# Performance work log

Hardware: AMD Instinct MI355X
Metric: run time of the kernel (lower is better)

## Reference

```python
import jax, jax.numpy as jnp
import numpy as np

B, T, A = 64, 100, 8732          # batch, padded GT boxes per image, SSD300 anchors
NUM_CLASSES = 21                 # VOC
THR = 0.5                        # overlap_threshold
VAR0, VAR1 = 0.1, 0.2            # loc_variance


def setup_inputs() -> dict:
    key = jax.random.key(0)
    k1, k2, k3, k4, k5 = jax.random.split(key, 5)
    # GT boxes: valid point-coord boxes in [0,1] with positive area, plus float label col
    xy1 = jax.random.uniform(k1, (B, T, 2)) * 0.7
    wh = jax.random.uniform(k2, (B, T, 2)) * 0.28 + 0.02
    labels = jax.random.randint(k3, (B, T), 0, NUM_CLASSES - 1).astype(jnp.float32)
    targets = jnp.concatenate([xy1, xy1 + wh, labels[..., None]], axis=-1)  # [B,T,5]
    # anchors in center coords (cx, cy, w, h), positive w/h
    cxy = jax.random.uniform(k4, (A, 2))
    awh = jax.random.uniform(k5, (A, 2)) * 0.48 + 0.02
    anchors = jnp.concatenate([cxy, awh], axis=-1)  # [A,4]
    return {"targets": targets, "anchors": anchors}


def _iou(boxes, anchors_pt):
    # boxes [T,4] point coords, anchors_pt [A,4] point coords -> [T,A]
    tl = jnp.maximum(boxes[:, None, :2], anchors_pt[None, :, :2])
    br = jnp.minimum(boxes[:, None, 2:], anchors_pt[None, :, 2:])
    inter = jnp.prod(jnp.clip(br - tl, 0.0), axis=-1)
    area_b = jnp.prod(boxes[:, 2:] - boxes[:, :2], axis=-1)
    area_a = jnp.prod(anchors_pt[:, 2:] - anchors_pt[:, :2], axis=-1)
    return inter / (area_b[:, None] + area_a[None, :] - inter)


def reference(targets, anchors):
    # centerCoordsToPointCoords(anchors)
    anchors_pt = jnp.concatenate(
        [anchors[:, :2] - anchors[:, 2:] * 0.5, anchors[:, :2] + anchors[:, 2:] * 0.5],
        axis=-1,
    )

    def match(tgt):  # tgt: [T,5]
        boxes = tgt[:, :4]
        labels = tgt[:, 4]
        iou = _iou(boxes, anchors_pt)                    # [T,A]
        anchor_index = jnp.argmax(iou, axis=1)           # best anchor per GT [T]
        gt_overlap = jnp.max(iou, axis=0)                # best GT overlap per anchor [A]
        gt_index = jnp.argmax(iou, axis=0)               # best GT per anchor [A]
        # index_fill_: guarantee each GT's best anchor counts as matched
        gt_overlap = gt_overlap.at[anchor_index].set(1.0)
        gt_index = gt_index.at[anchor_index].set(jnp.arange(boxes.shape[0]))
        matched = boxes[gt_index]                        # [A,4] point coords
        # pointCoordsToCenterCoords + encodeCenterCoords
        cxy = (matched[:, :2] + matched[:, 2:]) * 0.5
        wh = matched[:, 2:] - matched[:, :2]
        loc = jnp.concatenate(
            [(cxy - anchors[:, :2]) / (VAR0 * anchors[:, 2:]),
             jnp.log(wh / anchors[:, 2:]) / VAR1],
            axis=-1,
        )                                                # [A,4]
        conf = (labels[gt_index] + 1.0).astype(jnp.int32)
        conf = jnp.where(gt_overlap < THR, 0, conf)      # background below threshold
        return loc, conf

    return jax.vmap(match)(targets)  # loc_t [B,A,4], conf_t [B,A]
```

## Files before the change

### kernel.cpp

```cpp
#include <hip/hip_runtime.h>

#define BB 64
#define TT 100
#define TSPLIT 52
#define AA 8732
#define CHUNK 512
#define NCHUNK ((AA + CHUNK - 1) / CHUNK)

typedef unsigned long long u64;
typedef unsigned int u32;
typedef unsigned short u16;

__device__ __forceinline__ float fdiv_faithful(float i, float u) {
    float r = __builtin_amdgcn_rcpf(u);
    r = __builtin_fmaf(__builtin_fmaf(-u, r, 1.0f), r, r);
    float q = __fmul_rn(i, r);
    float rem = __builtin_fmaf(-u, q, i);
    return __builtin_fmaf(rem, r, q);
}

__device__ __forceinline__ float iou_f(float bx1, float by1, float bx2, float by2, float areab,
                                       float ax1, float ay1, float ax2, float ay2, float areaa) {
    float dx = fmaxf(__fsub_rn(fminf(bx2, ax2), fmaxf(bx1, ax1)), 0.0f);
    float dy = fmaxf(__fsub_rn(fminf(by2, ay2), fmaxf(by1, ay1)), 0.0f);
    float inter = __fmul_rn(dx, dy);
    float uni = __fsub_rn(__fadd_rn(areab, areaa), inter);
    return fdiv_faithful(inter, uni);
}

__device__ __forceinline__ void wave_max63_x4(float& x0, float& x1, float& x2, float& x3) {
#define DPP4(ctrl)                                                                              \
    {                                                                                           \
        int t0 = __builtin_amdgcn_update_dpp(__float_as_int(x0), __float_as_int(x0), (ctrl), 0xf, 0xf, false); \
        int t1 = __builtin_amdgcn_update_dpp(__float_as_int(x1), __float_as_int(x1), (ctrl), 0xf, 0xf, false); \
        int t2 = __builtin_amdgcn_update_dpp(__float_as_int(x2), __float_as_int(x2), (ctrl), 0xf, 0xf, false); \
        int t3 = __builtin_amdgcn_update_dpp(__float_as_int(x3), __float_as_int(x3), (ctrl), 0xf, 0xf, false); \
        x0 = fmaxf(x0, __int_as_float(t0));                                                     \
        x1 = fmaxf(x1, __int_as_float(t1));                                                     \
        x2 = fmaxf(x2, __int_as_float(t2));                                                     \
        x3 = fmaxf(x3, __int_as_float(t3));                                                     \
    }
    DPP4(0x111)
    DPP4(0x112)
    DPP4(0x114)
    DPP4(0x118)
    DPP4(0x142)
    DPP4(0x143)
#undef DPP4
}

__global__ __launch_bounds__(256) void k_init(u64* __restrict__ keys) {
    int i = blockIdx.x * 256 + threadIdx.x;
    if (i < BB * TT) keys[i] = 0ULL;
}

__global__ __launch_bounds__(512) void k_phaseA(const float* __restrict__ targets,
                                                const float* __restrict__ anchors,
                                                u64* __restrict__ keys,
                                                u16* __restrict__ pa) {
    const int b = blockIdx.y;
    const int tid = threadIdx.x;
    const int half = tid >> 8;
    const int u = tid & 255;
    const int a0 = blockIdx.x * CHUNK + u * 2;
    const bool valid = a0 < AA;
    const int lane = tid & 63, wv = tid >> 6;

    __shared__ float4 sh_box[TT];
    __shared__ __align__(16) float sh_area[TT];
    __shared__ u64 sh_red[4][TT];
    __shared__ u64 sh_pa[CHUNK];

    if (tid < TT) {
        const float* tg = targets + ((size_t)b * TT + tid) * 5;
        float x1 = tg[0], y1 = tg[1], x2 = tg[2], y2 = tg[3];
        sh_box[tid] = make_float4(x1, y1, x2, y2);
        sh_area[tid] = __fmul_rn(__fsub_rn(x2, x1), __fsub_rn(y2, y1));
    }
    __syncthreads();

    float ax10 = 0.f, ay10 = 0.f, ax20 = 0.f, ay20 = 0.f, aa0 = 1.f;
    float ax11 = 0.f, ay11 = 0.f, ax21 = 0.f, ay21 = 0.f, aa1 = 1.f;
    if (valid) {
        const float4* anc = (const float4*)(anchors + (size_t)a0 * 4);
        float4 c0 = anc[0], c1 = anc[1];
        float hx0 = __fmul_rn(c0.z, 0.5f), hy0 = __fmul_rn(c0.w, 0.5f);
        ax10 = __fsub_rn(c0.x, hx0); ay10 = __fsub_rn(c0.y, hy0);
        ax20 = __fadd_rn(c0.x, hx0); ay20 = __fadd_rn(c0.y, hy0);
        aa0 = __fmul_rn(__fsub_rn(ax20, ax10), __fsub_rn(ay20, ay10));
        float hx1 = __fmul_rn(c1.z, 0.5f), hy1 = __fmul_rn(c1.w, 0.5f);
        ax11 = __fsub_rn(c1.x, hx1); ay11 = __fsub_rn(c1.y, hy1);
        ax21 = __fadd_rn(c1.x, hx1); ay21 = __fadd_rn(c1.y, hy1);
        aa1 = __fmul_rn(__fsub_rn(ax21, ax11), __fsub_rn(ay21, ay11));
    }

    float best0 = -1.f, best1 = -1.f;
    int gi0 = 0, gi1 = 0;
    const u32 wave_base = (u32)blockIdx.x * CHUNK + (u32)(wv & 3) * 128u;

    const int tbeg = half ? TSPLIT : 0;
    const int tend = half ? TT : TSPLIT;
    for (int t = tbeg; t < tend; t += 4) {
        float4 B0 = sh_box[t + 0], B1 = sh_box[t + 1];
        float4 B2 = sh_box[t + 2], B3 = sh_box[t + 3];
        const float4 arv = *(const float4*)&sh_area[t];
        float ar0 = arv.x, ar1 = arv.y, ar2 = arv.z, ar3 = arv.w;

        float v00 = iou_f(B0.x, B0.y, B0.z, B0.w, ar0, ax10, ay10, ax20, ay20, aa0);
        float v01 = iou_f(B0.x, B0.y, B0.z, B0.w, ar0, ax11, ay11, ax21, ay21, aa1);
        float v10 = iou_f(B1.x, B1.y, B1.z, B1.w, ar1, ax10, ay10, ax20, ay20, aa0);
        float v11 = iou_f(B1.x, B1.y, B1.z, B1.w, ar1, ax11, ay11, ax21, ay21, aa1);
        float v20 = iou_f(B2.x, B2.y, B2.z, B2.w, ar2, ax10, ay10, ax20, ay20, aa0);
        float v21 = iou_f(B2.x, B2.y, B2.z, B2.w, ar2, ax11, ay11, ax21, ay21, aa1);
        float v30 = iou_f(B3.x, B3.y, B3.z, B3.w, ar3, ax10, ay10, ax20, ay20, aa0);
        float v31 = iou_f(B3.x, B3.y, B3.z, B3.w, ar3, ax11, ay11, ax21, ay21, aa1);

        if (v00 > best0) { best0 = v00; gi0 = t; }
        if (v10 > best0) { best0 = v10; gi0 = t + 1; }
        if (v20 > best0) { best0 = v20; gi0 = t + 2; }
        if (v30 > best0) { best0 = v30; gi0 = t + 3; }
        if (v01 > best1) { best1 = v01; gi1 = t; }
        if (v11 > best1) { best1 = v11; gi1 = t + 1; }
        if (v21 > best1) { best1 = v21; gi1 = t + 2; }
        if (v31 > best1) { best1 = v31; gi1 = t + 3; }

        float vm0 = fmaxf(v00, v01), vm1 = fmaxf(v10, v11);
        float vm2 = fmaxf(v20, v21), vm3 = fmaxf(v30, v31);
        float w0 = vm0, w1 = vm1, w2 = vm2, w3 = vm3;
        wave_max63_x4(w0, w1, w2, w3);
        u32 wm0 = (u32)__builtin_amdgcn_readlane(__float_as_int(w0), 63);
        u32 wm1 = (u32)__builtin_amdgcn_readlane(__float_as_int(w1), 63);
        u32 wm2 = (u32)__builtin_amdgcn_readlane(__float_as_int(w2), 63);
        u32 wm3 = (u32)__builtin_amdgcn_readlane(__float_as_int(w3), 63);
        u64 me0 = __ballot(vm0 == __uint_as_float(wm0));
        u64 mp0 = __ballot(v01 > v00);
        u64 me1 = __ballot(vm1 == __uint_as_float(wm1));
        u64 mp1 = __ballot(v11 > v10);
        u64 me2 = __ballot(vm2 == __uint_as_float(wm2));
        u64 mp2 = __ballot(v21 > v20);
        u64 me3 = __ballot(vm3 == __uint_as_float(wm3));
        u64 mp3 = __ballot(v31 > v30);
        u32 wl0 = (u32)(__ffsll((long long)me0) - 1);
        u32 wl1 = (u32)(__ffsll((long long)me1) - 1);
        u32 wl2 = (u32)(__ffsll((long long)me2) - 1);
        u32 wl3 = (u32)(__ffsll((long long)me3) - 1);
        u32 g0 = wave_base + wl0 * 2u + (u32)((mp0 >> wl0) & 1ULL);
        u32 g1 = wave_base + wl1 * 2u + (u32)((mp1 >> wl1) & 1ULL);
        u32 g2 = wave_base + wl2 * 2u + (u32)((mp2 >> wl2) & 1ULL);
        u32 g3 = wave_base + wl3 * 2u + (u32)((mp3 >> wl3) & 1ULL);
        if (lane == 0) {
            u64* r = &sh_red[wv & 3][t];
            r[0] = (((u64)wm0) << 32) | (u32)~g0;
            r[1] = (((u64)wm1) << 32) | (u32)~g1;
            r[2] = (((u64)wm2) << 32) | (u32)~g2;
            r[3] = (((u64)wm3) << 32) | (u32)~g3;
        }
    }
    __syncthreads();

    if (tid < TT) {
        u64 m0 = sh_red[0][tid], m1 = sh_red[1][tid];
        u64 m2 = sh_red[2][tid], m3 = sh_red[3][tid];
        u64 m = m0 > m1 ? m0 : m1;
        if (m2 > m) m = m2;
        if (m3 > m) m = m3;
        atomicMax(&keys[b * TT + tid], m);
    }

    if (half == 0) {
        sh_pa[u * 2 + 0] = (((u64)__float_as_uint(best0)) << 32) | (u32)(~(u32)gi0);
        sh_pa[u * 2 + 1] = (((u64)__float_as_uint(best1)) << 32) | (u32)(~(u32)gi1);
    }
    __syncthreads();
    if (half == 1 && valid) {
        u64 k0 = (((u64)__float_as_uint(best0)) << 32) | (u32)(~(u32)gi0);
        u64 k1 = (((u64)__float_as_uint(best1)) << 32) | (u32)(~(u32)gi1);
        u64 m0 = sh_pa[u * 2 + 0]; if (k0 > m0) m0 = k0;
        u64 m1 = sh_pa[u * 2 + 1]; if (k1 > m1) m1 = k1;
        u32 gA0 = (~(u32)m0) & 0x7Fu;
        u32 gA1 = (~(u32)m1) & 0x7Fu;
        float bv0 = __uint_as_float((u32)(m0 >> 32));
        float bv1 = __uint_as_float((u32)(m1 >> 32));
        u32 f0 = gA0 | (bv0 >= 0.5f ? 0x80u : 0u);
        u32 f1 = gA1 | (bv1 >= 0.5f ? 0x80u : 0u);
        *(u32*)(pa + (size_t)b * AA + a0) = f0 | (f1 << 16);
    }
}

__global__ __launch_bounds__(256) void k_encode(const float* __restrict__ targets,
                                                const float* __restrict__ anchors,
                                                const u64* __restrict__ keys,
                                                const u16* __restrict__ pa,
                                                float* __restrict__ out) {
    const int b = blockIdx.y;
    const int a = blockIdx.x * 256 + threadIdx.x;

    __shared__ float sh_t[TT][6];
    __shared__ u32 sh_ov[256];

    sh_ov[threadIdx.x] = 0;
    __syncthreads();
    for (int t = threadIdx.x; t < TT; t += 256) {
        const float* tg = targets + ((size_t)b * TT + t) * 5;
        sh_t[t][0] = tg[0]; sh_t[t][1] = tg[1];
        sh_t[t][2] = tg[2]; sh_t[t][3] = tg[3];
        sh_t[t][4] = tg[4];
        u32 at = ~(u32)(keys[b * TT + t] & 0xFFFFFFFFu);
        if ((at >> 8) == (u32)blockIdx.x)
            atomicMax(&sh_ov[at & 255], 0x100u | (u32)t);
    }
    __syncthreads();
    if (a >= AA) return;

    u32 ov = sh_ov[threadIdx.x];
    u32 v = pa[(size_t)b * AA + a];
    int gi; bool pos;
    if (ov) { gi = (int)(ov & 0x7F); pos = true; }
    else     { gi = (int)(v & 0x7F); pos = (v & 0x80) != 0; }

    const float4 anc = *(const float4*)(anchors + (size_t)a * 4);
    const float mx1 = sh_t[gi][0], my1 = sh_t[gi][1], mx2 = sh_t[gi][2], my2 = sh_t[gi][3];
    const float cx = (mx1 + mx2) * 0.5f, cy = (my1 + my2) * 0.5f;
    const float w = mx2 - mx1, h = my2 - my1;
    const float l0 = (cx - anc.x) / (0.1f * anc.z);
    const float l1 = (cy - anc.y) / (0.1f * anc.w);
    const float l2 = logf(w / anc.z) / 0.2f;
    const float l3 = logf(h / anc.w) / 0.2f;

    const size_t base = ((size_t)b * AA + a) * 4;
    *(float4*)(out + base) = make_float4(l0, l1, l2, l3);
    float conf = pos ? (float)(int)(sh_t[gi][4] + 1.0f) : 0.0f;
    out[(size_t)BB * AA * 4 + (size_t)b * AA + a] = conf;
}

extern "C" void kernel_launch(void* const* d_in, const int* in_sizes, int n_in,
                              void* d_out, int out_size, void* d_ws, size_t ws_size,
                              hipStream_t stream) {
    const float* targets = (const float*)d_in[0];
    const float* anchors = (const float*)d_in[1];
    float* out = (float*)d_out;
    u64* keys = (u64*)d_ws;
    u16* pa = (u16*)((char*)d_ws + (size_t)BB * TT * 8);

    k_init<<<(BB * TT + 255) / 256, 256, 0, stream>>>(keys);
    dim3 gA(NCHUNK, BB);
    k_phaseA<<<gA, 512, 0, stream>>>(targets, anchors, keys, pa);
    dim3 gE((AA + 255) / 256, BB);
    k_encode<<<gE, 256, 0, stream>>>(targets, anchors, keys, pa, out);
}
```

Before: 122.5 us.

## Split GT-box range across a second grid dimension and merge partial argmax in encode

```diff
diff --git a/kernel.cpp b/kernel.cpp
--- a/kernel.cpp
+++ b/kernel.cpp
@@ -2,7 +2,6 @@
 
 #define BB 64
 #define TT 100
-#define TSPLIT 52
 #define AA 8732
 #define CHUNK 512
 #define NCHUNK ((AA + CHUNK - 1) / CHUNK)
@@ -10,6 +9,8 @@
 typedef unsigned long long u64;
 typedef unsigned int u32;
 typedef unsigned short u16;
+
+__constant__ int c_tbl[5] = {0, 28, 52, 76, 100};
 
 __device__ __forceinline__ float fdiv_faithful(float i, float u) {
     float r = __builtin_amdgcn_rcpf(u);
@@ -57,8 +58,9 @@
 __global__ __launch_bounds__(512) void k_phaseA(const float* __restrict__ targets,
                                                 const float* __restrict__ anchors,
                                                 u64* __restrict__ keys,
-                                                u16* __restrict__ pa) {
+                                                u64* __restrict__ pa2) {
     const int b = blockIdx.y;
+    const int z = blockIdx.z;
     const int tid = threadIdx.x;
     const int half = tid >> 8;
     const int u = tid & 255;
@@ -98,8 +100,8 @@
     int gi0 = 0, gi1 = 0;
     const u32 wave_base = (u32)blockIdx.x * CHUNK + (u32)(wv & 3) * 128u;
 
-    const int tbeg = half ? TSPLIT : 0;
-    const int tend = half ? TT : TSPLIT;
+    const int tbeg = c_tbl[z * 2 + half];
+    const int tend = c_tbl[z * 2 + half + 1];
     for (int t = tbeg; t < tend; t += 4) {
         float4 B0 = sh_box[t + 0], B1 = sh_box[t + 1];
         float4 B2 = sh_box[t + 2], B3 = sh_box[t + 3];
@@ -158,7 +160,7 @@
     }
     __syncthreads();
 
-    if (tid < TT) {
+    if (tid >= c_tbl[z * 2] && tid < c_tbl[z * 2 + 2]) {
         u64 m0 = sh_red[0][tid], m1 = sh_red[1][tid];
         u64 m2 = sh_red[2][tid], m3 = sh_red[3][tid];
         u64 m = m0 > m1 ? m0 : m1;
@@ -177,21 +179,16 @@
         u64 k1 = (((u64)__float_as_uint(best1)) << 32) | (u32)(~(u32)gi1);
         u64 m0 = sh_pa[u * 2 + 0]; if (k0 > m0) m0 = k0;
         u64 m1 = sh_pa[u * 2 + 1]; if (k1 > m1) m1 = k1;
-        u32 gA0 = (~(u32)m0) & 0x7Fu;
-        u32 gA1 = (~(u32)m1) & 0x7Fu;
-        float bv0 = __uint_as_float((u32)(m0 >> 32));
-        float bv1 = __uint_as_float((u32)(m1 >> 32));
-        u32 f0 = gA0 | (bv0 >= 0.5f ? 0x80u : 0u);
-        u32 f1 = gA1 | (bv1 >= 0.5f ? 0x80u : 0u);
-        *(u32*)(pa + (size_t)b * AA + a0) = f0 | (f1 << 16);
+        pa2[((size_t)b * AA + a0) * 2 + z] = m0;
+        pa2[((size_t)b * AA + a0 + 1) * 2 + z] = m1;
     }
 }
 
 __global__ __launch_bounds__(256) void k_encode(const float* __restrict__ targets,
                                                 const float* __restrict__ anchors,
                                                 const u64* __restrict__ keys,
-                                                const u16* __restrict__ pa,
-                                                float* __restrict__ out) {
+                                                const u64* pa2,
+                                                float* out) {
     const int b = blockIdx.y;
     const int a = blockIdx.x * 256 + threadIdx.x;
 
@@ -212,11 +209,17 @@
     __syncthreads();
     if (a >= AA) return;
 
+    const u64* pc = pa2 + ((size_t)b * AA + a) * 2;
+    u64 kz0 = pc[0], kz1 = pc[1];
+    u64 m = kz0 > kz1 ? kz0 : kz1;
+
     u32 ov = sh_ov[threadIdx.x];
-    u32 v = pa[(size_t)b * AA + a];
     int gi; bool pos;
     if (ov) { gi = (int)(ov & 0x7F); pos = true; }
-    else     { gi = (int)(v & 0x7F); pos = (v & 0x80) != 0; }
+    else {
+        gi = (int)((~(u32)m) & 0x7F);
+        pos = __uint_as_float((u32)(m >> 32)) >= 0.5f;
+    }
 
     const float4 anc = *(const float4*)(anchors + (size_t)a * 4);
     const float mx1 = sh_t[gi][0], my1 = sh_t[gi][1], mx2 = sh_t[gi][2], my2 = sh_t[gi][3];
@@ -240,11 +243,11 @@
     const float* anchors = (const float*)d_in[1];
     float* out = (float*)d_out;
     u64* keys = (u64*)d_ws;
-    u16* pa = (u16*)((char*)d_ws + (size_t)BB * TT * 8);
+    u64* pa2 = (u64*)d_out;
 
     k_init<<<(BB * TT + 255) / 256, 256, 0, stream>>>(keys);
-    dim3 gA(NCHUNK, BB);
-    k_phaseA<<<gA, 512, 0, stream>>>(targets, anchors, keys, pa);
+    dim3 gA(NCHUNK, BB, 2);
+    k_phaseA<<<gA, 512, 0, stream>>>(targets, anchors, keys, pa2);
     dim3 gE((AA + 255) / 256, BB);
-    k_encode<<<gE, 256, 0, stream>>>(targets, anchors, keys, pa, out);
-}
+    k_encode<<<gE, 256, 0, stream>>>(targets, anchors, keys, pa2, out);
+}
```

Result: no change. 121.7 us (-0.6%).
